# Optimization experiments

Measured on AMD Instinct MI355X. Metric: run time of the kernel, lower is better.

Reference implementation:

```python
import jax, jax.numpy as jnp
import numpy as np

N = 5000
NFEAT = 512
NHID = 64
NHEADS = 8
NCLASS = 40
ALPHA = 0.2  # leaky relu slope
NEG_INF = -9e15


def setup_inputs() -> dict:
    key = jax.random.key(0)
    ks = jax.random.split(key, 12)
    x = jax.random.normal(ks[0], (N, NFEAT), dtype=jnp.float32)
    # binary adjacency, ~32 avg degree, with self loops
    adj = (jax.random.uniform(ks[1], (N, N)) < (32.0 / N)).astype(jnp.float32)
    adj = jnp.maximum(adj, jnp.eye(N, dtype=jnp.float32))
    s = 1.0 / np.sqrt(NFEAT)
    W_h = jax.random.uniform(ks[2], (NHEADS, NFEAT, NHID), minval=-s, maxval=s, dtype=jnp.float32)
    a_h = jax.random.uniform(ks[3], (NHEADS, 2 * NHID), minval=-s, maxval=s, dtype=jnp.float32)
    s2 = 1.0 / np.sqrt(NHID * NHEADS)
    W_o = jax.random.uniform(ks[4], (NHID * NHEADS, NHID), minval=-s2, maxval=s2, dtype=jnp.float32)
    a_o = jax.random.uniform(ks[5], (2 * NHID,), minval=-s2, maxval=s2, dtype=jnp.float32)
    s3 = 1.0 / np.sqrt(NHID)
    fc1_w = jax.random.uniform(ks[6], (NHID, 200), minval=-s3, maxval=s3, dtype=jnp.float32)
    fc1_b = jax.random.uniform(ks[7], (200,), minval=-s3, maxval=s3, dtype=jnp.float32)
    s4 = 1.0 / np.sqrt(200)
    fc2_w = jax.random.uniform(ks[8], (200, NCLASS), minval=-s4, maxval=s4, dtype=jnp.float32)
    fc2_b = jax.random.uniform(ks[9], (NCLASS,), minval=-s4, maxval=s4, dtype=jnp.float32)
    return {"x": x, "adj": adj, "W_h": W_h, "a_h": a_h, "W_o": W_o, "a_o": a_o,
            "fc1_w": fc1_w, "fc1_b": fc1_b, "fc2_w": fc2_w, "fc2_b": fc2_b}


def _masked_attention(e, adj):
    # e: [..., N, N]; mask where adj == 0, then row softmax
    e = jnp.where(adj > 0, e, NEG_INF)
    return jax.nn.softmax(e, axis=-1)


def reference(x, adj, W_h, a_h, W_o, a_o, fc1_w, fc1_b, fc2_w, fc2_b):
    # ---- multi-head GAT layer (concat=True), eval mode (dropout off) ----
    Wh = jnp.einsum('nf,hfo->hno', x, W_h)                 # [H, N, nhid]
    f1 = jnp.einsum('hno,ho->hn', Wh, a_h[:, :NHID])       # [H, N]
    f2 = jnp.einsum('hno,ho->hn', Wh, a_h[:, NHID:])       # [H, N]
    e = jax.nn.leaky_relu(f1[:, :, None] + f2[:, None, :], ALPHA)  # [H, N, N]
    att = _masked_attention(e, adj[None, :, :])
    h = jnp.einsum('hnm,hmo->hno', att, Wh)                # [H, N, nhid]
    h1 = jax.nn.elu(h).transpose(1, 0, 2).reshape(N, NHEADS * NHID)  # concat heads

    # ---- output GAT layer (concat=False) ----
    Wh2 = h1 @ W_o                                         # [N, nhid]
    g1 = Wh2 @ a_o[:NHID]                                  # [N]
    g2 = Wh2 @ a_o[NHID:]                                  # [N]
    e2 = jax.nn.leaky_relu(g1[:, None] + g2[None, :], ALPHA)
    att2 = _masked_attention(e2, adj)
    h2 = att2 @ Wh2                                        # [N, nhid]

    # ---- MLP head ----
    h3 = jax.nn.elu(h2 @ fc1_w + fc1_b)
    return h3 @ fc2_w + fc2_b                              # [N, nclass]
```

## Files before the change

### kernel.cpp

```cpp
#include <hip/hip_runtime.h>

typedef unsigned short u16;
typedef unsigned int u32;
typedef unsigned long long u64;
typedef __bf16 bf16_t;
typedef __bf16 bf16x8 __attribute__((ext_vector_type(8)));
typedef float f32x4 __attribute__((ext_vector_type(4)));
typedef u32 u32x4 __attribute__((ext_vector_type(4)));

#define NN 5000
#define NF 512
#define NH 64
#define HEADS 8
#define NCLS 40
#define CAP 128
#define LRELU 0.2f
#define BMW 80

#define CVT_BIG 320
#define BM_BLKS 1250
#define CVT_GRID (CVT_BIG + 8 + BM_BLKS)

__device__ __forceinline__ bool adj_is_bf16(const void* adj) {
    return ((*(const u32*)adj) & 0xFFFFu) != 0u;
}
__device__ __forceinline__ u16 rne_bf16(float f) {
    u32 u = __float_as_uint(f);
    u += 0x7FFFu + ((u >> 16) & 1u);
    return (u16)(u >> 16);
}
__device__ __forceinline__ float up_bf16(u16 h) {
    return __uint_as_float((u32)h << 16);
}
__device__ __forceinline__ u32x4 ntload4(const void* p, int idx) {
    return __builtin_nontemporal_load(((const u32x4*)p) + idx);
}

__global__ __launch_bounds__(256) void cvt(const void* __restrict__ x, const void* __restrict__ W_h,
                                           const void* __restrict__ adj,
                                           const void* a_h, const void* W_o, const void* a_o,
                                           const void* f1w, const void* f1b,
                                           const void* f2w, const void* f2b,
                                           u16* __restrict__ xc, u16* __restrict__ whc,
                                           float* a_hc, float* W_oc, float* a_oc,
                                           float* f1wc, float* f1bc, float* f2wc, float* f2bc,
                                           u64* __restrict__ bm) {
    const bool isb = adj_is_bf16(adj);
    const int b = blockIdx.x;
    if (b < CVT_BIG) {
        const int X4 = NN * NF / 4;
        const int T4 = X4 + HEADS * NF * NH / 4;
        for (int i = b * 256 + threadIdx.x; i < T4; i += CVT_BIG * 256) {
            const void* src; u16* dst; int off;
            if (i < X4) { src = x; dst = xc; off = i; }
            else        { src = W_h; dst = whc; off = i - X4; }
            ushort4 o;
            if (isb) {
                o = ((const ushort4*)src)[off];
            } else {
                u32x4 vv = ntload4(src, off);
                o.x = rne_bf16(__uint_as_float(vv[0])); o.y = rne_bf16(__uint_as_float(vv[1]));
                o.z = rne_bf16(__uint_as_float(vv[2])); o.w = rne_bf16(__uint_as_float(vv[3]));
            }
            ((ushort4*)dst)[off] = o;
        }
    } else if (b < CVT_BIG + 8) {
        const int s0 = HEADS * 2 * NH, s1 = HEADS * NH * NH, s2 = 2 * NH,
                  s3 = NH * 200, s4 = 200, s5 = 200 * NCLS, s6 = NCLS;
        const int total = s0 + s1 + s2 + s3 + s4 + s5 + s6;
        for (int i = (b - CVT_BIG) * 256 + threadIdx.x; i < total; i += 8 * 256) {
            const void* src; float* dst; int off = i;
            if (off < s0) { src = a_h; dst = a_hc; }
            else if ((off -= s0) < s1) { src = W_o;  dst = W_oc; }
            else if ((off -= s1) < s2) { src = a_o;  dst = a_oc; }
            else if ((off -= s2) < s3) { src = f1w;  dst = f1wc; }
            else if ((off -= s3) < s4) { src = f1b;  dst = f1bc; }
            else if ((off -= s4) < s5) { src = f2w;  dst = f2wc; }
            else { off -= s5;           src = f2b;  dst = f2bc; }
            dst[off] = isb ? up_bf16(((const u16*)src)[off]) : ((const float*)src)[off];
        }
    } else {
        const int lane = threadIdx.x & 63;
        const int wid  = threadIdx.x >> 6;
        const int r = (b - CVT_BIG - 8) * 4 + wid;
        u64* bmrow = bm + (size_t)r * BMW;
        if (!isb) {
            const float* row = (const float*)adj + (size_t)r * NN;
            #pragma unroll
            for (int pass = 0; pass < 2; ++pass) {
                u32x4 v[10];
                #pragma unroll
                for (int k = 0; k < 10; ++k) {
                    int c = (pass * 10 + k) * 64 + lane;
                    v[k] = (c < 1250) ? ntload4(row, c) : (u32x4){0u, 0u, 0u, 0u};
                }
                #pragma unroll
                for (int k = 0; k < 10; ++k) {
                    int i = pass * 10 + k;
                    #pragma unroll
                    for (int j = 0; j < 4; ++j) {
                        u64 m = __ballot(v[k][j] != 0u);
                        if (lane == j) bmrow[i * 4 + j] = m;
                    }
                }
            }
        } else {
            const u16* row = (const u16*)adj + (size_t)r * NN;
            u32x4 v[10];
            #pragma unroll
            for (int k = 0; k < 10; ++k) {
                int c = k * 64 + lane;
                v[k] = (c < 625) ? ntload4(row, c) : (u32x4){0u, 0u, 0u, 0u};
            }
            #pragma unroll
            for (int k = 0; k < 10; ++k) {
                #pragma unroll
                for (int j = 0; j < 4; ++j) {
                    u64 mlo = __ballot((v[k][j] & 0xFFFFu) != 0u);
                    u64 mhi = __ballot((v[k][j] >> 16) != 0u);
                    if (lane == 2 * j)     bmrow[k * 8 + 2 * j]     = mlo;
                    if (lane == 2 * j + 1) bmrow[k * 8 + 2 * j + 1] = mhi;
                }
            }
        }
    }
}

__global__ __launch_bounds__(256) void gemm1_f(const bf16_t* __restrict__ x,
                                               const bf16_t* __restrict__ W_h,
                                               const float* __restrict__ a_h,
                                               float* __restrict__ Wh,
                                               float* __restrict__ f1,
                                               float* __restrict__ f2) {
    const int lane = threadIdx.x & 63;
    const int wid  = threadIdx.x >> 6;
    const int rg = blockIdx.x;
    const int h  = blockIdx.y;
    const int quad = lane >> 4;
    const int lr   = lane & 15;
    const int kq   = quad * 8;
    const int nCol = wid * 16 + lr;
    const bf16_t* Bh = W_h + (size_t)h * NF * NH;
    __shared__ float f1s[4][64], f2s[4][64];

    bf16x8 bfrag[16];
    #pragma unroll
    for (int s = 0; s < 16; ++s) {
        bf16x8 bb;
        #pragma unroll
        for (int j = 0; j < 8; ++j) bb[j] = Bh[(s * 32 + kq + j) * NH + nCol];
        bfrag[s] = bb;
    }
    const float a1c = a_h[h * 128 + nCol];
    const float a2c = a_h[h * 128 + NH + nCol];

    for (int t = 0; t < 4; ++t) {
        const int rb = rg * 64 + t * 16;
        int row  = rb + lr;
        int rowc = row < NN ? row : NN - 1;
        const bf16_t* xp = x + (size_t)rowc * NF + kq;
        f32x4 acc = {0.f, 0.f, 0.f, 0.f};
        #pragma unroll
        for (int s = 0; s < 16; ++s) {
            bf16x8 a = *(const bf16x8*)(xp + s * 32);
            acc = __builtin_amdgcn_mfma_f32_16x16x32_bf16(a, bfrag[s], acc, 0, 0, 0);
        }
        #pragma unroll
        for (int r = 0; r < 4; ++r) {
            int gr = rb + quad * 4 + r;
            if (gr < NN) Wh[(size_t)gr * (HEADS * NH) + h * NH + nCol] = acc[r];
            float p1 = acc[r] * a1c, p2 = acc[r] * a2c;
            #pragma unroll
            for (int o = 8; o; o >>= 1) { p1 += __shfl_xor(p1, o); p2 += __shfl_xor(p2, o); }
            if (lr == 0) { f1s[wid][t * 16 + quad * 4 + r] = p1; f2s[wid][t * 16 + quad * 4 + r] = p2; }
        }
    }
    __syncthreads();
    if (wid == 0) {
        int gr = rg * 64 + lane;
        if (gr < NN) {
            f1[h * NN + gr] = f1s[0][lane] + f1s[1][lane] + f1s[2][lane] + f1s[3][lane];
            f2[h * NN + gr] = f2s[0][lane] + f2s[1][lane] + f2s[2][lane] + f2s[3][lane];
        }
    }
}

__global__ __launch_bounds__(256) void agg1f(const void* __restrict__ adj,
                                             const u64* __restrict__ bm,
                                             const float* __restrict__ Wh,
                                             const float* __restrict__ f1,
                                             const float* __restrict__ f2,
                                             int* __restrict__ nbr, int* __restrict__ deg,
                                             float* __restrict__ h1) {
    const bool isb = adj_is_bf16(adj);
    const int lane = threadIdx.x & 63;
    const int wid  = threadIdx.x >> 6;
    const int n = blockIdx.x;
    __shared__ int s_nbr[CAP];
    __shared__ int s_dall;

    if (wid == 0) {
        const u64* bmrow = bm + (size_t)n * BMW;
        int base = 0;
        #pragma unroll
        for (int r2 = 0; r2 < 2; ++r2) {
            int w = r2 * 64 + lane;
            u64 mw = (w < BMW) ? bmrow[w] : 0ull;
            int pc = __popcll(mw);
            int scan = pc;
            #pragma unroll
            for (int o = 1; o < 64; o <<= 1) {
                int t = __shfl_up(scan, o);
                if (lane >= o) scan += t;
            }
            int off = base + scan - pc;
            while (mw) {
                int bb = __ffsll(mw) - 1;
                mw &= mw - 1;
                int elem;
                if (!isb) elem = ((w >> 2) * 64 + bb) * 4 + (w & 3);
                else      elem = ((w >> 3) * 64 + bb) * 8 + (w & 7);
                if (off < CAP) s_nbr[off] = elem;
                ++off;
            }
            base += __shfl(scan, 63);
        }
        if (lane == 0) s_dall = base < CAP ? base : CAP;
    }
    __syncthreads();
    const int dall = s_dall;
    for (int i = threadIdx.x; i < dall; i += 256) nbr[(size_t)n * CAP + i] = s_nbr[i];
    if (threadIdx.x == 0) deg[n] = dall;

    const int ha = wid, hb = wid + 4;
    const int nb0 = (lane < dall) ? s_nbr[lane] : 0;
    const int nb1 = (lane + 64 < dall) ? s_nbr[lane + 64] : 0;
    const float f10 = f1[ha * NN + n], f11 = f1[hb * NN + n];
    const float* f2ha = f2 + (size_t)ha * NN;
    const float* f2hb = f2 + (size_t)hb * NN;

    float e00 = -INFINITY, e01 = -INFINITY, e10 = -INFINITY, e11 = -INFINITY;
    if (lane < dall) {
        float a = f10 + f2ha[nb0]; e00 = a > 0.f ? a : LRELU * a;
        float b = f11 + f2hb[nb0]; e10 = b > 0.f ? b : LRELU * b;
    }
    if (lane + 64 < dall) {
        float a = f10 + f2ha[nb1]; e01 = a > 0.f ? a : LRELU * a;
        float b = f11 + f2hb[nb1]; e11 = b > 0.f ? b : LRELU * b;
    }
    float mx0 = fmaxf(e00, e01), mx1 = fmaxf(e10, e11);
    #pragma unroll
    for (int o = 32; o; o >>= 1) {
        mx0 = fmaxf(mx0, __shfl_xor(mx0, o));
        mx1 = fmaxf(mx1, __shfl_xor(mx1, o));
    }
    float p00 = lane < dall ? expf(e00 - mx0) : 0.f;
    float p01 = lane + 64 < dall ? expf(e01 - mx0) : 0.f;
    float p10 = lane < dall ? expf(e10 - mx1) : 0.f;
    float p11 = lane + 64 < dall ? expf(e11 - mx1) : 0.f;
    float sm0 = p00 + p01, sm1 = p10 + p11;
    #pragma unroll
    for (int o = 32; o; o >>= 1) { sm0 += __shfl_xor(sm0, o); sm1 += __shfl_xor(sm1, o); }

    float A0 = 0.f, A1 = 0.f, A2 = 0.f, A3 = 0.f;
    float B0 = 0.f, B1 = 0.f, B2 = 0.f, B3 = 0.f;
    const float* W0 = Wh + ha * NH + lane;
    const float* W1 = Wh + hb * NH + lane;
    int j = 0;
    for (; j + 4 <= dall; j += 4) {
        #pragma unroll
        for (int i = 0; i < 4; ++i) {
            int jj = j + i;
            int sl = jj & 63;
            bool lo = jj < 64;
            int   m  = lo ? __shfl(nb0, sl) : __shfl(nb1, sl);
            float a0 = lo ? __shfl(p00, sl) : __shfl(p01, sl);
            float a1 = lo ? __shfl(p10, sl) : __shfl(p11, sl);
            size_t base = (size_t)m * (HEADS * NH);
            float w0 = W0[base], w1 = W1[base];
            if (i == 0) { A0 += a0 * w0; B0 += a1 * w1; }
            else if (i == 1) { A1 += a0 * w0; B1 += a1 * w1; }
            else if (i == 2) { A2 += a0 * w0; B2 += a1 * w1; }
            else { A3 += a0 * w0; B3 += a1 * w1; }
        }
    }
    for (; j < dall; ++j) {
        int sl = j & 63;
        bool lo = j < 64;
        int   m  = lo ? __shfl(nb0, sl) : __shfl(nb1, sl);
        float a0 = lo ? __shfl(p00, sl) : __shfl(p01, sl);
        float a1 = lo ? __shfl(p10, sl) : __shfl(p11, sl);
        size_t base = (size_t)m * (HEADS * NH);
        A0 += a0 * W0[base]; B0 += a1 * W1[base];
    }
    float hv0 = (A0 + A1 + A2 + A3) / sm0;
    float hv1 = (B0 + B1 + B2 + B3) / sm1;
    hv0 = hv0 > 0.f ? hv0 : expf(hv0) - 1.f;
    hv1 = hv1 > 0.f ? hv1 : expf(hv1) - 1.f;
    h1[(size_t)n * (HEADS * NH) + ha * NH + lane] = hv0;
    h1[(size_t)n * (HEADS * NH) + hb * NH + lane] = hv1;
}

__global__ __launch_bounds__(256) void gemm2_4(const float* __restrict__ h1,
                                               const float* __restrict__ W_o,
                                               const float* __restrict__ a_o,
                                               float* __restrict__ Wh2,
                                               float* __restrict__ g1,
                                               float* __restrict__ g2) {
    const int t = threadIdx.x;
    const int n0 = blockIdx.x * 4;
    __shared__ float sh[4 * 512];
    __shared__ float ps[4][4][64];
    const float4* src = (const float4*)(h1 + (size_t)n0 * 512);
    ((float4*)sh)[t]       = src[t];
    ((float4*)sh)[t + 256] = src[t + 256];
    __syncthreads();
    const int o = t & 63, part = t >> 6;
    float a0 = 0.f, a1 = 0.f, a2 = 0.f, a3 = 0.f;
    const float* wo = W_o + part * 128 * 64 + o;
    const float* s0 = sh + part * 128;
    #pragma unroll 4
    for (int f = 0; f < 128; ++f) {
        float w = wo[f * 64];
        a0 += s0[f] * w; a1 += s0[512 + f] * w; a2 += s0[1024 + f] * w; a3 += s0[1536 + f] * w;
    }
    ps[part][0][o] = a0; ps[part][1][o] = a1; ps[part][2][o] = a2; ps[part][3][o] = a3;
    __syncthreads();
    const int nd = t >> 6;
    float w2 = ps[0][nd][o] + ps[1][nd][o] + ps[2][nd][o] + ps[3][nd][o];
    Wh2[(size_t)(n0 + nd) * 64 + o] = w2;
    float p1 = w2 * a_o[o], p2 = w2 * a_o[64 + o];
    #pragma unroll
    for (int s = 32; s; s >>= 1) { p1 += __shfl_xor(p1, s); p2 += __shfl_xor(p2, s); }
    if (o == 0) { g1[n0 + nd] = p1; g2[n0 + nd] = p2; }
}

__global__ __launch_bounds__(256) void agg2_mlp(const float* __restrict__ Wh2,
                                                const float* __restrict__ g1,
                                                const float* __restrict__ g2,
                                                const int* __restrict__ nbr,
                                                const int* __restrict__ deg,
                                                const float* __restrict__ fc1_w,
                                                const float* __restrict__ fc1_b,
                                                const float* __restrict__ fc2_w,
                                                const float* __restrict__ fc2_b,
                                                float* __restrict__ out) {
    const int lane = threadIdx.x & 63;
    const int wid  = threadIdx.x >> 6;
    const int t = threadIdx.x;
    const int n0 = blockIdx.x * 4;
    const int n = n0 + wid;
    __shared__ float s_alpha[4][CAP];
    __shared__ int   s_nbr[4][CAP];
    __shared__ float s_h2[4][NH];
    __shared__ float s_h3[4][200];
    __shared__ float ps2[2][4][NCLS];
    const int d = deg[n];
    const int* nb = nbr + (size_t)n * CAP;
    const float gn = g1[n];

    float mx = -INFINITY;
    for (int j = lane; j < d; j += 64) {
        int m = nb[j];
        s_nbr[wid][j] = m;
        float e = gn + g2[m];
        e = e > 0.f ? e : LRELU * e;
        s_alpha[wid][j] = e;
        mx = fmaxf(mx, e);
    }
    #pragma unroll
    for (int o = 32; o; o >>= 1) mx = fmaxf(mx, __shfl_xor(mx, o));
    float sm = 0.f;
    for (int j = lane; j < d; j += 64) {
        float p = expf(s_alpha[wid][j] - mx);
        s_alpha[wid][j] = p;
        sm += p;
    }
    #pragma unroll
    for (int o = 32; o; o >>= 1) sm += __shfl_xor(sm, o);

    float acc0 = 0.f, acc1 = 0.f, acc2 = 0.f, acc3 = 0.f;
    int j = 0;
    for (; j + 4 <= d; j += 4) {
        acc0 += s_alpha[wid][j]     * Wh2[(size_t)s_nbr[wid][j]     * NH + lane];
        acc1 += s_alpha[wid][j + 1] * Wh2[(size_t)s_nbr[wid][j + 1] * NH + lane];
        acc2 += s_alpha[wid][j + 2] * Wh2[(size_t)s_nbr[wid][j + 2] * NH + lane];
        acc3 += s_alpha[wid][j + 3] * Wh2[(size_t)s_nbr[wid][j + 3] * NH + lane];
    }
    for (; j < d; ++j) acc0 += s_alpha[wid][j] * Wh2[(size_t)s_nbr[wid][j] * NH + lane];
    s_h2[wid][lane] = (acc0 + acc1 + acc2 + acc3) / sm;
    __syncthreads();

    if (t < 200) {
        float b0 = 0.f, b1 = 0.f, b2 = 0.f, b3 = 0.f;
        #pragma unroll 4
        for (int f = 0; f < NH; ++f) {
            float w = fc1_w[f * 200 + t];
            b0 += s_h2[0][f] * w; b1 += s_h2[1][f] * w; b2 += s_h2[2][f] * w; b3 += s_h2[3][f] * w;
        }
        float bb = fc1_b[t];
        b0 += bb; b1 += bb; b2 += bb; b3 += bb;
        s_h3[0][t] = b0 > 0.f ? b0 : expf(b0) - 1.f;
        s_h3[1][t] = b1 > 0.f ? b1 : expf(b1) - 1.f;
        s_h3[2][t] = b2 > 0.f ? b2 : expf(b2) - 1.f;
        s_h3[3][t] = b3 > 0.f ? b3 : expf(b3) - 1.f;
    }
    __syncthreads();

    if (t < 80) {
        const int o = t % 40, fh = t / 40;
        float c0 = 0.f, c1 = 0.f, c2 = 0.f, c3 = 0.f;
        #pragma unroll 4
        for (int f = fh * 100; f < fh * 100 + 100; ++f) {
            float w = fc2_w[f * NCLS + o];
            c0 += s_h3[0][f] * w; c1 += s_h3[1][f] * w; c2 += s_h3[2][f] * w; c3 += s_h3[3][f] * w;
        }
        ps2[fh][0][o] = c0; ps2[fh][1][o] = c1; ps2[fh][2][o] = c2; ps2[fh][3][o] = c3;
    }
    __syncthreads();
    if (t < 160) {
        const int nd = t / 40, o = t % 40;
        out[(size_t)(n0 + nd) * NCLS + o] = ps2[0][nd][o] + ps2[1][nd][o] + fc2_b[o];
    }
}

extern "C" void kernel_launch(void* const* d_in, const int* in_sizes, int n_in,
                              void* d_out, int out_size, void* d_ws, size_t ws_size,
                              hipStream_t stream) {
    const void* x     = d_in[0];
    const void* adj   = d_in[1];
    const void* W_h   = d_in[2];
    const void* a_h   = d_in[3];
    const void* W_o   = d_in[4];
    const void* a_o   = d_in[5];
    const void* fc1_w = d_in[6];
    const void* fc1_b = d_in[7];
    const void* fc2_w = d_in[8];
    const void* fc2_b = d_in[9];
    float* out = (float*)d_out;

    char* ws = (char*)d_ws;
    int*   nbr   = (int*)(ws + 0);
    int*   deg   = (int*)(ws + 2560000);
    float* Wh    = (float*)(ws + 2580000);
    float* f1    = (float*)(ws + 12820000);
    float* f2    = (float*)(ws + 12980000);
    float* h1    = (float*)(ws + 13140000);
    float* Wh2   = (float*)(ws + 23380000);
    float* g1    = (float*)(ws + 24660000);
    float* g2    = (float*)(ws + 24680000);
    u16*   xc    = (u16*)(ws + 24700000);
    u16*   whc   = (u16*)(ws + 29820000);
    float* a_hc  = (float*)(ws + 30344288);
    float* W_oc  = (float*)(ws + 30348384);
    float* a_oc  = (float*)(ws + 30479456);
    float* f1wc  = (float*)(ws + 30479968);
    float* f1bc  = (float*)(ws + 30531168);
    float* f2wc  = (float*)(ws + 30531968);
    float* f2bc  = (float*)(ws + 30563968);
    u64*   bm    = (u64*)(ws + 30564128);

    cvt<<<CVT_GRID, 256, 0, stream>>>(x, W_h, adj, a_h, W_o, a_o,
                                      fc1_w, fc1_b, fc2_w, fc2_b,
                                      xc, whc, a_hc, W_oc, a_oc,
                                      f1wc, f1bc, f2wc, f2bc, bm);
    gemm1_f<<<dim3(79, HEADS), 256, 0, stream>>>((const bf16_t*)xc, (const bf16_t*)whc,
                                                 a_hc, Wh, f1, f2);
    agg1f<<<NN, 256, 0, stream>>>(adj, bm, Wh, f1, f2, nbr, deg, h1);
    gemm2_4<<<NN / 4, 256, 0, stream>>>(h1, W_oc, a_oc, Wh2, g1, g2);
    agg2_mlp<<<NN / 4, 256, 0, stream>>>(Wh2, g1, g2, nbr, deg,
                                         f1wc, f1bc, f2wc, f2bc, out);
}
```

Measured before the change: 277.2 us.

## Pre-swizzle W_h into MFMA fragment layout, move bitmask build into gemm1, stage probabilities in LDS

The conversion kernel now writes W_h in the exact bf16x8 fragment order the MFMA B operand uses, so gemm1 loads each fragment with one vector load instead of eight strided scalar loads. The adjacency bitmask construction moves out of the cvt kernel into extra blocks of the gemm1 launch, so it runs alongside the GEMM. In agg1f, normalised attention weights and neighbour indices are read from shared memory instead of broadcast by shuffles, the softmax division is folded in beforehand, and the aggregation loop is unrolled by 8. The scattered 2-byte writes during conversion and the extra LDS use are the costs traded against the removed shuffles and strided loads.

Result: faster. 271.6 us (-2.0%).

```diff
diff --git a/kernel.cpp b/kernel.cpp
--- a/kernel.cpp
+++ b/kernel.cpp
@@ -18,8 +18,9 @@
 #define BMW 80
 
 #define CVT_BIG 320
+#define CVT_GRID (CVT_BIG + 8)
 #define BM_BLKS 1250
-#define CVT_GRID (CVT_BIG + 8 + BM_BLKS)
+#define G1_BLKS (79 * HEADS)
 
 __device__ __forceinline__ bool adj_is_bf16(const void* adj) {
     return ((*(const u32*)adj) & 0xFFFFu) != 0u;
@@ -43,28 +44,47 @@
                                            const void* f2w, const void* f2b,
                                            u16* __restrict__ xc, u16* __restrict__ whc,
                                            float* a_hc, float* W_oc, float* a_oc,
-                                           float* f1wc, float* f1bc, float* f2wc, float* f2bc,
-                                           u64* __restrict__ bm) {
+                                           float* f1wc, float* f1bc, float* f2wc, float* f2bc) {
     const bool isb = adj_is_bf16(adj);
     const int b = blockIdx.x;
     if (b < CVT_BIG) {
         const int X4 = NN * NF / 4;
         const int T4 = X4 + HEADS * NF * NH / 4;
         for (int i = b * 256 + threadIdx.x; i < T4; i += CVT_BIG * 256) {
-            const void* src; u16* dst; int off;
-            if (i < X4) { src = x; dst = xc; off = i; }
-            else        { src = W_h; dst = whc; off = i - X4; }
-            ushort4 o;
-            if (isb) {
-                o = ((const ushort4*)src)[off];
+            if (i < X4) {
+                ushort4 o;
+                if (isb) {
+                    o = ((const ushort4*)x)[i];
+                } else {
+                    u32x4 vv = ntload4(x, i);
+                    o.x = rne_bf16(__uint_as_float(vv[0])); o.y = rne_bf16(__uint_as_float(vv[1]));
+                    o.z = rne_bf16(__uint_as_float(vv[2])); o.w = rne_bf16(__uint_as_float(vv[3]));
+                }
+                ((ushort4*)xc)[i] = o;
             } else {
-                u32x4 vv = ntload4(src, off);
-                o.x = rne_bf16(__uint_as_float(vv[0])); o.y = rne_bf16(__uint_as_float(vv[1]));
-                o.z = rne_bf16(__uint_as_float(vv[2])); o.w = rne_bf16(__uint_as_float(vv[3]));
-            }
-            ((ushort4*)dst)[off] = o;
-        }
-    } else if (b < CVT_BIG + 8) {
+                const int iw = i - X4;
+                u16 q[4];
+                if (isb) {
+                    ushort4 vv = ((const ushort4*)W_h)[iw];
+                    q[0] = vv.x; q[1] = vv.y; q[2] = vv.z; q[3] = vv.w;
+                } else {
+                    u32x4 vv = ntload4(W_h, iw);
+                    q[0] = rne_bf16(__uint_as_float(vv[0])); q[1] = rne_bf16(__uint_as_float(vv[1]));
+                    q[2] = rne_bf16(__uint_as_float(vv[2])); q[3] = rne_bf16(__uint_as_float(vv[3]));
+                }
+                const int e0 = iw * 4;
+                const int h = e0 >> 15;
+                const int rem = e0 & 32767;
+                const int f = rem >> 6, o0 = rem & 63;
+                const int base = (h * 16 + (f >> 5)) * 2048 + ((f >> 3) & 3) * 128 + (f & 7);
+                #pragma unroll
+                for (int k = 0; k < 4; ++k) {
+                    const int o = o0 + k;
+                    whc[base + (o >> 4) * 512 + (o & 15) * 8] = q[k];
+                }
+            }
+        }
+    } else {
         const int s0 = HEADS * 2 * NH, s1 = HEADS * NH * NH, s2 = 2 * NH,
                   s3 = NH * 200, s4 = 200, s5 = 200 * NCLS, s6 = NCLS;
         const int total = s0 + s1 + s2 + s3 + s4 + s5 + s6;
@@ -79,10 +99,24 @@
             else { off -= s5;           src = f2b;  dst = f2bc; }
             dst[off] = isb ? up_bf16(((const u16*)src)[off]) : ((const float*)src)[off];
         }
-    } else {
-        const int lane = threadIdx.x & 63;
-        const int wid  = threadIdx.x >> 6;
-        const int r = (b - CVT_BIG - 8) * 4 + wid;
+    }
+}
+
+__global__ __launch_bounds__(256) void gemm1_f(const bf16_t* __restrict__ x,
+                                               const bf16_t* __restrict__ Wf,
+                                               const float* __restrict__ a_h,
+                                               const void* __restrict__ adj,
+                                               u64* __restrict__ bm,
+                                               float* __restrict__ Wh,
+                                               float* __restrict__ f1,
+                                               float* __restrict__ f2) {
+    const int lane = threadIdx.x & 63;
+    const int wid  = threadIdx.x >> 6;
+    const int b = blockIdx.x;
+
+    if (b >= G1_BLKS) {
+        const bool isb = adj_is_bf16(adj);
+        const int r = (b - G1_BLKS) * 4 + wid;
         u64* bmrow = bm + (size_t)r * BMW;
         if (!isb) {
             const float* row = (const float*)adj + (size_t)r * NN;
@@ -123,34 +157,22 @@
                 }
             }
         }
-    }
-}
-
-__global__ __launch_bounds__(256) void gemm1_f(const bf16_t* __restrict__ x,
-                                               const bf16_t* __restrict__ W_h,
-                                               const float* __restrict__ a_h,
-                                               float* __restrict__ Wh,
-                                               float* __restrict__ f1,
-                                               float* __restrict__ f2) {
-    const int lane = threadIdx.x & 63;
-    const int wid  = threadIdx.x >> 6;
-    const int rg = blockIdx.x;
-    const int h  = blockIdx.y;
+        return;
+    }
+
+    const int rg = b % 79;
+    const int h  = b / 79;
     const int quad = lane >> 4;
     const int lr   = lane & 15;
     const int kq   = quad * 8;
     const int nCol = wid * 16 + lr;
-    const bf16_t* Bh = W_h + (size_t)h * NF * NH;
     __shared__ float f1s[4][64], f2s[4][64];
 
+    const bf16_t* Bf = Wf + (size_t)h * (16 * 2048) + threadIdx.x * 8;
     bf16x8 bfrag[16];
     #pragma unroll
-    for (int s = 0; s < 16; ++s) {
-        bf16x8 bb;
-        #pragma unroll
-        for (int j = 0; j < 8; ++j) bb[j] = Bh[(s * 32 + kq + j) * NH + nCol];
-        bfrag[s] = bb;
-    }
+    for (int s = 0; s < 16; ++s) bfrag[s] = *(const bf16x8*)(Bf + s * 2048);
+
     const float a1c = a_h[h * 128 + nCol];
     const float a2c = a_h[h * 128 + NH + nCol];
 
@@ -198,6 +220,7 @@
     const int n = blockIdx.x;
     __shared__ int s_nbr[CAP];
     __shared__ int s_dall;
+    __shared__ float s_p0[4][CAP], s_p1[4][CAP];
 
     if (wid == 0) {
         const u64* bmrow = bm + (size_t)n * BMW;
@@ -262,39 +285,35 @@
     #pragma unroll
     for (int o = 32; o; o >>= 1) { sm0 += __shfl_xor(sm0, o); sm1 += __shfl_xor(sm1, o); }
 
+    const float i0 = 1.f / sm0, i1 = 1.f / sm1;
+    s_p0[wid][lane] = p00 * i0; s_p0[wid][lane + 64] = p01 * i0;
+    s_p1[wid][lane] = p10 * i1; s_p1[wid][lane + 64] = p11 * i1;
+
     float A0 = 0.f, A1 = 0.f, A2 = 0.f, A3 = 0.f;
     float B0 = 0.f, B1 = 0.f, B2 = 0.f, B3 = 0.f;
     const float* W0 = Wh + ha * NH + lane;
     const float* W1 = Wh + hb * NH + lane;
     int j = 0;
-    for (; j + 4 <= dall; j += 4) {
+    for (; j + 8 <= dall; j += 8) {
         #pragma unroll
-        for (int i = 0; i < 4; ++i) {
-            int jj = j + i;
-            int sl = jj & 63;
-            bool lo = jj < 64;
-            int   m  = lo ? __shfl(nb0, sl) : __shfl(nb1, sl);
-            float a0 = lo ? __shfl(p00, sl) : __shfl(p01, sl);
-            float a1 = lo ? __shfl(p10, sl) : __shfl(p11, sl);
-            size_t base = (size_t)m * (HEADS * NH);
+        for (int u = 0; u < 8; ++u) {
+            float a0 = s_p0[wid][j + u];
+            float a1 = s_p1[wid][j + u];
+            size_t base = (size_t)s_nbr[j + u] * (HEADS * NH);
             float w0 = W0[base], w1 = W1[base];
-            if (i == 0) { A0 += a0 * w0; B0 += a1 * w1; }
-            else if (i == 1) { A1 += a0 * w0; B1 += a1 * w1; }
-            else if (i == 2) { A2 += a0 * w0; B2 += a1 * w1; }
-            else { A3 += a0 * w0; B3 += a1 * w1; }
+            if ((u & 3) == 0)      { A0 += a0 * w0; B0 += a1 * w1; }
+            else if ((u & 3) == 1) { A1 += a0 * w0; B1 += a1 * w1; }
+            else if ((u & 3) == 2) { A2 += a0 * w0; B2 += a1 * w1; }
+            else                   { A3 += a0 * w0; B3 += a1 * w1; }
         }
     }
     for (; j < dall; ++j) {
-        int sl = j & 63;
-        bool lo = j < 64;
-        int   m  = lo ? __shfl(nb0, sl) : __shfl(nb1, sl);
-        float a0 = lo ? __shfl(p00, sl) : __shfl(p01, sl);
-        float a1 = lo ? __shfl(p10, sl) : __shfl(p11, sl);
-        size_t base = (size_t)m * (HEADS * NH);
+        float a0 = s_p0[wid][j], a1 = s_p1[wid][j];
+        size_t base = (size_t)s_nbr[j] * (HEADS * NH);
         A0 += a0 * W0[base]; B0 += a1 * W1[base];
     }
-    float hv0 = (A0 + A1 + A2 + A3) / sm0;
-    float hv1 = (B0 + B1 + B2 + B3) / sm1;
+    float hv0 = A0 + A1 + A2 + A3;
+    float hv1 = B0 + B1 + B2 + B3;
     hv0 = hv0 > 0.f ? hv0 : expf(hv0) - 1.f;
     hv1 = hv1 > 0.f ? hv1 : expf(hv1) - 1.f;
     h1[(size_t)n * (HEADS * NH) + ha * NH + lane] = hv0;
@@ -463,9 +482,9 @@
     cvt<<<CVT_GRID, 256, 0, stream>>>(x, W_h, adj, a_h, W_o, a_o,
                                       fc1_w, fc1_b, fc2_w, fc2_b,
                                       xc, whc, a_hc, W_oc, a_oc,
-                                      f1wc, f1bc, f2wc, f2bc, bm);
-    gemm1_f<<<dim3(79, HEADS), 256, 0, stream>>>((const bf16_t*)xc, (const bf16_t*)whc,
-                                                 a_hc, Wh, f1, f2);
+                                      f1wc, f1bc, f2wc, f2bc);
+    gemm1_f<<<G1_BLKS + BM_BLKS, 256, 0, stream>>>((const bf16_t*)xc, (const bf16_t*)whc,
+                                                   a_hc, adj, bm, Wh, f1, f2);
     agg1f<<<NN, 256, 0, stream>>>(adj, bm, Wh, f1, f2, nbr, deg, h1);
     gemm2_4<<<NN / 4, 256, 0, stream>>>(h1, W_oc, a_oc, Wh2, g1, g2);
     agg2_mlp<<<NN / 4, 256, 0, stream>>>(Wh2, g1, g2, nbr, deg,
```
